# Performance work log

Hardware: AMD Instinct MI355X
Metric: run time of the kernel (lower is better)

## Reference

```python
import jax, jax.numpy as jnp
import numpy as np

ALPHA = 0.2        # LeakyReLU negative slope
NEG = -9e15        # mask value used by the torch module
N, FIN, H, D = 4096, 20, 4, 64


def gat_layer(h, adj_mask, W, a_src, a_dst, average):
    """Multi-head GAT layer. W: [H,Fin,Fout], a_src/a_dst: [H,Fout].
    e_ij = LeakyReLU(a_src . Wh_i + a_dst . Wh_j) == a^T [Wh_i || Wh_j],
    identical math to the N x N x 2F concat in the torch code, without
    materializing the pairwise concat tensor."""
    Wh = jnp.einsum('nf,hfo->hno', h, W)                 # [H,N,F]
    f_s = jnp.einsum('hno,ho->hn', Wh, a_src)            # [H,N]
    f_d = jnp.einsum('hno,ho->hn', Wh, a_dst)            # [H,N]
    e = jax.nn.leaky_relu(f_s[:, :, None] + f_d[:, None, :], ALPHA)  # [H,N,N]
    e = jnp.where(adj_mask[None], e, NEG)
    att = jax.nn.softmax(e, axis=-1)
    out = jax.nn.elu(jnp.einsum('hnm,hmo->hno', att, Wh))  # per-head ELU (concat=True inside)
    if average:
        return out.mean(axis=0)                           # [N,F]
    return jnp.transpose(out, (1, 0, 2)).reshape(h.shape[0], -1)  # [N,H*F]


def setup_inputs() -> dict:
    key = jax.random.key(0)
    ks = jax.random.split(key, 6)
    x = jax.random.normal(ks[0], (N, FIN), jnp.float32)
    adj = jax.random.randint(ks[1], (N, N), 0, 2, jnp.int32)
    # layer 0: 20 -> 64 per head, 4 heads, concat -> 256
    W0 = jax.random.normal(ks[2], (H, FIN, D), jnp.float32) * 0.3
    a0 = jax.random.normal(ks[3], (H, 2 * D), jnp.float32) * 0.1
    # layer 1: 256 -> 64 per head, heads averaged
    W1 = jax.random.normal(ks[4], (H, H * D, D), jnp.float32) * 0.06
    a1 = jax.random.normal(ks[5], (H, 2 * D), jnp.float32) * 0.1
    return {"x": x, "adj": adj, "W0": W0, "a0": a0, "W1": W1, "a1": a1}


def reference(x, adj, W0, a0, W1, a1):
    mask = adj > 0
    h = gat_layer(x, mask, W0, a0[:, :D], a0[:, D:], average=False)   # [N, 256]
    return gat_layer(h, mask, W1, a1[:, :D], a1[:, D:], average=True)  # [N, 64]
```

## Files before the change

### kernel.cpp

```cpp
#include <hip/hip_runtime.h>
#include <hip/hip_fp16.h>
#include <math.h>

#define NN 4096
#define FIN 20
#define NH 4
#define DH 64
#define ALPHA 0.2f
#define LOG2E 1.4426950408889634f

typedef _Float16 f16x8 __attribute__((ext_vector_type(8)));
typedef _Float16 f16x4 __attribute__((ext_vector_type(4)));
typedef __fp16 fp16x2 __attribute__((ext_vector_type(2)));
typedef float f32x4 __attribute__((ext_vector_type(4)));

#if defined(__has_builtin)
#if __has_builtin(__builtin_amdgcn_exp2f)
#define FEXP2(x) __builtin_amdgcn_exp2f(x)
#endif
#endif
#ifndef FEXP2
extern "C" __device__ float __ocml_native_exp2_f32(float);
#define FEXP2(x) __ocml_native_exp2_f32(x)
#endif

__device__ inline void gload_lds16(const void* gsrc, void* ldsbase) {
    __builtin_amdgcn_global_load_lds(
        (const __attribute__((address_space(1))) void*)gsrc,
        (__attribute__((address_space(3))) void*)ldsbase, 16, 0, 0);
}

__global__ __launch_bounds__(256) void k_pack(const int* __restrict__ adj,
        unsigned char* __restrict__ bits) {
    int t = blockIdx.x * 256 + threadIdx.x;
    const int4* p = (const int4*)(adj + (size_t)t * 8);
    int4 a = p[0], b = p[1];
    unsigned int byte = 0;
    byte |= (a.x > 0) << 0; byte |= (a.y > 0) << 1;
    byte |= (a.z > 0) << 2; byte |= (a.w > 0) << 3;
    byte |= (b.x > 0) << 4; byte |= (b.y > 0) << 5;
    byte |= (b.z > 0) << 6; byte |= (b.w > 0) << 7;
    bits[t] = (unsigned char)byte;
}

__global__ __launch_bounds__(256) void k_l0wh(const float* __restrict__ x,
        const float* __restrict__ W0, const float* __restrict__ a0,
        _Float16* __restrict__ whT, float* __restrict__ fs, float* __restrict__ fd) {
    __shared__ float xs[16 * FIN];
    int n0 = blockIdx.x * 16;
    int tid = threadIdx.x;
    for (int i = tid; i < 16 * FIN; i += 256) xs[i] = x[n0 * FIN + i];
    __syncthreads();
    int h = tid >> 6, d = tid & 63;
    float w0r[FIN];
#pragma unroll
    for (int f = 0; f < FIN; ++f) w0r[f] = W0[(h * FIN + f) * DH + d];
    float asrc = a0[h * 2 * DH + d];
    float adst = a0[h * 2 * DH + DH + d];
    f16x8 wv[2];
#pragma unroll
    for (int n = 0; n < 16; ++n) {
        float wh = 0.f;
#pragma unroll
        for (int f = 0; f < FIN; ++f) wh = fmaf(xs[n * FIN + f], w0r[f], wh);
        wv[n >> 3][n & 7] = (_Float16)wh;
        float sv = wh * asrc, dv = wh * adst;
#pragma unroll
        for (int off = 1; off <= 32; off <<= 1) {
            sv += __shfl_xor(sv, off);
            dv += __shfl_xor(dv, off);
        }
        if (d == 0) { fs[h * NN + n0 + n] = sv; fd[h * NN + n0 + n] = dv; }
    }
    _Float16* dst = whT + ((size_t)(h * DH + d) * NN + n0);
    *(f16x8*)(dst) = wv[0];
    *(f16x8*)(dst + 8) = wv[1];
}

__global__ __launch_bounds__(256) void k_fdmax(const float* __restrict__ fd,
        float* __restrict__ fdm) {
    int h = blockIdx.x, tid = threadIdx.x;
    float m = -3e38f;
    for (int i = tid; i < NN; i += 256) m = fmaxf(m, fd[h * NN + i]);
#pragma unroll
    for (int off = 1; off <= 32; off <<= 1) m = fmaxf(m, __shfl_xor(m, off));
    __shared__ float mx[4];
    if ((tid & 63) == 0) mx[tid >> 6] = m;
    __syncthreads();
    if (tid == 0) fdm[h] = fmaxf(fmaxf(mx[0], mx[1]), fmaxf(mx[2], mx[3]));
}

__global__ void k_w1t(const float* __restrict__ W1, _Float16* __restrict__ w1T) {
    int u = blockIdx.x * 256 + threadIdx.x;
    int h = u >> 14, f = (u >> 6) & 255, d = u & 63;
    w1T[((size_t)(h * DH + d) << 8) + f] = (_Float16)W1[u];
}

__global__ __launch_bounds__(512) void k_attn(const float* __restrict__ fs,
        const float* __restrict__ fd, const float* __restrict__ fdmax,
        const _Float16* __restrict__ whT, const unsigned char* __restrict__ bits,
        float* __restrict__ pv, float* __restrict__ pl) {
    __shared__ __align__(16) char smem[34304];
    const int ch = blockIdx.x & 1;
    const int rowblk = (blockIdx.x >> 1) & 63;
    const int h = blockIdx.x >> 7;
    const int row0 = rowblk << 6;
    const int cb0 = ch << 11;
    const int tid = threadIdx.x;
    const int l = tid & 63, w = tid >> 6;
    const int rl = l & 15, g = l >> 4;
    const int rg = w >> 2, cq = w & 3;
    const int r0 = row0 + rg * 32 + rl;
    const int r1 = r0 + 16;
    const float fsr0 = fs[h * NN + r0], fsr1 = fs[h * NN + r1];
    const float fm = fdmax[h];
    const float su0 = fsr0 + fm, su1 = fsr1 + fm;
    const float m0 = fmaxf(su0, ALPHA * su0);
    const float m1 = fmaxf(su1, ALPHA * su1);
    const float A0 = (fsr0 - m0) * LOG2E, B0 = (ALPHA * fsr0 - m0) * LOG2E;
    const float A1 = (fsr1 - m1) * LOG2E, B1 = (ALPHA * fsr1 - m1) * LOG2E;
    const float* fdp = fd + h * NN + cb0 + cq * 32 + g * 8;
    const unsigned char* bp0 = bits + (size_t)r0 * (NN / 8) + (cb0 >> 3) + cq * 4;
    const unsigned char* bp1 = bits + (size_t)r1 * (NN / 8) + (cb0 >> 3) + cq * 4;
    const _Float16* whb = whT + (size_t)h * DH * NN + cb0;

    const int d0_ = tid >> 4, c0_ = tid & 15;
    const int d1_ = 32 + (tid >> 4), c1_ = tid & 15;
    const _Float16* src0 = whb + (size_t)d0_ * NN + 8 * (c0_ ^ (d0_ & 15));
    const _Float16* src1 = whb + (size_t)d1_ * NN + 8 * (c1_ ^ (d1_ & 15));
    char* dstA0 = smem + w * 1024;
    char* dstA1 = smem + 8192 + w * 1024;
    char* dstB0 = smem + 16384 + w * 1024;
    char* dstB1 = smem + 16384 + 8192 + w * 1024;

    f32x4 acc0[4] = {{0,0,0,0},{0,0,0,0},{0,0,0,0},{0,0,0,0}};
    f32x4 acc1[4] = {{0,0,0,0},{0,0,0,0},{0,0,0,0},{0,0,0,0}};
    f32x4 al0 = {0,0,0,0}, al1 = {0,0,0,0};
    f16x8 ones;
#pragma unroll
    for (int i = 0; i < 8; ++i) ones[i] = (_Float16)1.0f;
    const int rdswz = ((((cq << 2) | g) ^ rl) << 4);

    gload_lds16(src0, dstA0);
    gload_lds16(src1, dstA1);
    float4 faA = *(const float4*)(fdp);
    float4 fbA = *(const float4*)(fdp + 4);
    unsigned int mA0 = *(const unsigned int*)(bp0);
    unsigned int mA1 = *(const unsigned int*)(bp1);
    float4 faB, fbB;
    unsigned int mB0, mB1;
    __syncthreads();

#define COMPUTE(BUF, FA, FB, M0v, M1v)                                          \
    {                                                                           \
        const float fv[8] = {FA.x, FA.y, FA.z, FA.w, FB.x, FB.y, FB.z, FB.w};   \
        f16x8 av0, av1;                                                         \
        const int sh = g << 3;                                                  \
        _Pragma("unroll")                                                       \
        for (int i = 0; i < 8; i += 2) {                                        \
            float ta = fmaxf(fmaf(fv[i], LOG2E, A0), fmaf(fv[i], ALPHA * LOG2E, B0)); \
            ta = ((M0v >> (sh + i)) & 1u) ? ta : -1e30f;                        \
            float tb = fmaxf(fmaf(fv[i+1], LOG2E, A0), fmaf(fv[i+1], ALPHA * LOG2E, B0)); \
            tb = ((M0v >> (sh + i + 1)) & 1u) ? tb : -1e30f;                    \
            fp16x2 p0 = __builtin_amdgcn_cvt_pkrtz(FEXP2(ta), FEXP2(tb));       \
            av0[i] = (_Float16)p0[0]; av0[i+1] = (_Float16)p0[1];               \
            float tc = fmaxf(fmaf(fv[i], LOG2E, A1), fmaf(fv[i], ALPHA * LOG2E, B1)); \
            tc = ((M1v >> (sh + i)) & 1u) ? tc : -1e30f;                        \
            float td = fmaxf(fmaf(fv[i+1], LOG2E, A1), fmaf(fv[i+1], ALPHA * LOG2E, B1)); \
            td = ((M1v >> (sh + i + 1)) & 1u) ? td : -1e30f;                    \
            fp16x2 p1 = __builtin_amdgcn_cvt_pkrtz(FEXP2(tc), FEXP2(td));       \
            av1[i] = (_Float16)p1[0]; av1[i+1] = (_Float16)p1[1];               \
        }                                                                       \
        al0 = __builtin_amdgcn_mfma_f32_16x16x32_f16(av0, ones, al0, 0, 0, 0);  \
        al1 = __builtin_amdgcn_mfma_f32_16x16x32_f16(av1, ones, al1, 0, 0, 0);  \
        _Pragma("unroll")                                                       \
        for (int t4 = 0; t4 < 4; ++t4) {                                        \
            f16x8 bv = *(const f16x8*)((BUF) + ((16 * t4 + rl) << 8) + rdswz);  \
            acc0[t4] = __builtin_amdgcn_mfma_f32_16x16x32_f16(av0, bv, acc0[t4], 0, 0, 0); \
            acc1[t4] = __builtin_amdgcn_mfma_f32_16x16x32_f16(av1, bv, acc1[t4], 0, 0, 0); \
        }                                                                       \
    }

#pragma unroll 1
    for (int k = 0; k < 8; ++k) {
        const int tB = 2 * k + 1;
        gload_lds16(src0 + tB * 128, dstB0);
        gload_lds16(src1 + tB * 128, dstB1);
        faB = *(const float4*)(fdp + tB * 128);
        fbB = *(const float4*)(fdp + tB * 128 + 4);
        mB0 = *(const unsigned int*)(bp0 + tB * 16);
        mB1 = *(const unsigned int*)(bp1 + tB * 16);
        COMPUTE(smem, faA, fbA, mA0, mA1);
        __syncthreads();
        if (k < 7) {
            const int tA = 2 * k + 2;
            gload_lds16(src0 + tA * 128, dstA0);
            gload_lds16(src1 + tA * 128, dstA1);
            faA = *(const float4*)(fdp + tA * 128);
            fbA = *(const float4*)(fdp + tA * 128 + 4);
            mA0 = *(const unsigned int*)(bp0 + tA * 16);
            mA1 = *(const unsigned int*)(bp1 + tA * 16);
        }
        COMPUTE((smem + 16384), faB, fbB, mB0, mB1);
        __syncthreads();
    }
#undef COMPUTE

    float* red = (float*)smem;
    float* lred = (float*)(smem + 33792);
#pragma unroll
    for (int p = 0; p < 2; ++p) {
        if (rg == p) {
#pragma unroll
            for (int t4 = 0; t4 < 4; ++t4)
#pragma unroll
                for (int i = 0; i < 4; ++i) {
                    red[(cq * 32 + 4 * g + i) * 66 + 16 * t4 + rl]      = acc0[t4][i];
                    red[(cq * 32 + 16 + 4 * g + i) * 66 + 16 * t4 + rl] = acc1[t4][i];
                }
            if (rl == 0) {
#pragma unroll
                for (int i = 0; i < 4; ++i) {
                    lred[cq * 32 + 4 * g + i]      = al0[i];
                    lred[cq * 32 + 16 + 4 * g + i] = al1[i];
                }
            }
        }
        __syncthreads();
#pragma unroll
        for (int j = 0; j < 4; ++j) {
            const int R = w * 4 + j;
            float v = 0.f, L = 0.f;
#pragma unroll
            for (int cc = 0; cc < 4; ++cc) {
                v += red[(cc * 32 + R) * 66 + l];
                L += lred[cc * 32 + R];
            }
            const int Rg = row0 + p * 32 + R;
            pv[(((size_t)(ch * NH + h) * NN) + Rg) * 64 + l] = v;
            if (l == 0) pl[(size_t)(ch * NH + h) * NN + Rg] = L;
        }
        __syncthreads();
    }
}

template<int MODE>
__global__ __launch_bounds__(256) void k_merge(const float* __restrict__ pv,
        const float* __restrict__ pl, void* __restrict__ outp) {
    int t = blockIdx.x * 256 + threadIdx.x;
    if (MODE == 0) {
        int d = t & 63, n = (t >> 6) & (NN - 1), h = t >> 18;
        float v = pv[((size_t)h * NN + n) * 64 + d] + pv[((size_t)(NH + h) * NN + n) * 64 + d];
        float L = pl[h * NN + n] + pl[NH * NN + h * NN + n];
        float o = v * __builtin_amdgcn_rcpf(L);
        o = o > 0.f ? o : __expf(o) - 1.f;
        ((_Float16*)outp)[(size_t)n * (NH * DH) + h * DH + d] = (_Float16)o;
    } else {
        int d = t & 63, n = t >> 6;
        float s = 0.f;
#pragma unroll
        for (int h = 0; h < NH; ++h) {
            float v = pv[((size_t)h * NN + n) * 64 + d] + pv[((size_t)(NH + h) * NN + n) * 64 + d];
            float L = pl[h * NN + n] + pl[NH * NN + h * NN + n];
            float o = v * __builtin_amdgcn_rcpf(L);
            s += o > 0.f ? o : __expf(o) - 1.f;
        }
        ((float*)outp)[t] = 0.25f * s;
    }
}

__global__ __launch_bounds__(256) void k_l1wh(const _Float16* __restrict__ h16,
        const _Float16* __restrict__ w1T, const float* __restrict__ a1,
        _Float16* __restrict__ whT, float* __restrict__ fs, float* __restrict__ fd) {
    __shared__ float red[4][16][64];
    __shared__ _Float16 lt[16][64];
    int h = blockIdx.x >> 8;
    int row0 = (blockIdx.x & 255) << 4;
    int tid = threadIdx.x;
    int l = tid & 63, w = tid >> 6;
    int rl = l & 15, g = l >> 4;
    f32x4 acc[4] = {{0,0,0,0},{0,0,0,0},{0,0,0,0},{0,0,0,0}};
    const _Float16* ap = h16 + (size_t)(row0 + rl) * (NH * DH) + w * 64;
    const _Float16* bp = w1T + ((size_t)h * DH << 8) + w * 64;
#pragma unroll
    for (int j = 0; j < 2; ++j) {
        int fb = j * 32 + 8 * g;
        f16x8 avv = *(const f16x8*)(ap + fb);
#pragma unroll
        for (int t4 = 0; t4 < 4; ++t4) {
            f16x8 bv = *(const f16x8*)(bp + ((size_t)(16 * t4 + rl) << 8) + fb);
            acc[t4] = __builtin_amdgcn_mfma_f32_16x16x32_f16(avv, bv, acc[t4], 0, 0, 0);
        }
    }
#pragma unroll
    for (int t4 = 0; t4 < 4; ++t4)
#pragma unroll
        for (int i = 0; i < 4; ++i) red[w][t4 * 4 + i][l] = acc[t4][i];
    __syncthreads();
#pragma unroll
    for (int i = 0; i < 4; ++i) {
        float v = red[0][w * 4 + i][l] + red[1][w * 4 + i][l]
                + red[2][w * 4 + i][l] + red[3][w * 4 + i][l];
        lt[4 * g + i][16 * w + rl] = (_Float16)v;
    }
    __syncthreads();
    int d = tid & 63, rb = tid >> 6;
    f16x4 o;
#pragma unroll
    for (int j = 0; j < 4; ++j) o[j] = lt[rb * 4 + j][d];
    *(f16x4*)(whT + (size_t)(h * DH + d) * NN + row0 + rb * 4) = o;
    float as_ = a1[h * 2 * DH + d], ad_ = a1[h * 2 * DH + DH + d];
    float svj[4], dvj[4];
#pragma unroll
    for (int j = 0; j < 4; ++j) {
        float wv = (float)lt[rb * 4 + j][d];
        svj[j] = wv * as_;
        dvj[j] = wv * ad_;
    }
#pragma unroll
    for (int off = 1; off <= 32; off <<= 1) {
#pragma unroll
        for (int j = 0; j < 4; ++j) {
            svj[j] += __shfl_xor(svj[j], off);
            dvj[j] += __shfl_xor(dvj[j], off);
        }
    }
    if (d == 0) {
#pragma unroll
        for (int j = 0; j < 4; ++j) {
            fs[h * NN + row0 + rb * 4 + j] = svj[j];
            fd[h * NN + row0 + rb * 4 + j] = dvj[j];
        }
    }
}

extern "C" void kernel_launch(void* const* d_in, const int* in_sizes, int n_in,
                              void* d_out, int out_size, void* d_ws, size_t ws_size,
                              hipStream_t stream) {
    const float* x  = (const float*)d_in[0];
    const int* adj  = (const int*)d_in[1];
    const float* W0 = (const float*)d_in[2];
    const float* a0 = (const float*)d_in[3];
    const float* W1 = (const float*)d_in[4];
    const float* a1 = (const float*)d_in[5];
    float* out = (float*)d_out;
    char* ws = (char*)d_ws;

    unsigned char* bits = (unsigned char*)(ws);
    _Float16* whT0 = (_Float16*)(ws + (2ull << 20));
    _Float16* h16  = (_Float16*)(ws + (4ull << 20));
    _Float16* w1T  = (_Float16*)(ws + (6ull << 20));
    _Float16* whT1 = (_Float16*)(ws + (6ull << 20) + (256ull << 10));
    float* fs0  = (float*)(ws + (9ull << 20));
    float* fd0  = fs0 + NH * NN;
    float* fs1  = fd0 + NH * NN;
    float* fd1  = fs1 + NH * NN;
    float* fdm0 = fd1 + NH * NN;
    float* fdm1 = fdm0 + 8;
    float* pv   = (float*)(ws + (10ull << 20));
    float* pl   = (float*)(ws + (18ull << 20));

    k_pack<<<NN * NN / 8 / 256, 256, 0, stream>>>(adj, bits);
    k_w1t<<<(NH * NH * DH * DH) / 256, 256, 0, stream>>>(W1, w1T);
    k_l0wh<<<NN / 16, 256, 0, stream>>>(x, W0, a0, whT0, fs0, fd0);
    k_fdmax<<<NH, 256, 0, stream>>>(fd0, fdm0);
    k_attn<<<2 * NH * (NN / 64), 512, 0, stream>>>(fs0, fd0, fdm0, whT0, bits, pv, pl);
    k_merge<0><<<(NH * NN * DH) / 256, 256, 0, stream>>>(pv, pl, h16);
    k_l1wh<<<NH * (NN / 16), 256, 0, stream>>>(h16, w1T, a1, whT1, fs1, fd1);
    k_fdmax<<<NH, 256, 0, stream>>>(fd1, fdm1);
    k_attn<<<2 * NH * (NN / 64), 512, 0, stream>>>(fs1, fd1, fdm1, whT1, bits, pv, pl);
    k_merge<1><<<(NN * DH) / 256, 256, 0, stream>>>(pv, pl, out);
}
```

Measured before the change: 110.8 us.

## Split attention columns four ways and fuse front-end kernels into one launch

After: 128.1 us. 1.16x slower.

```diff
diff --git a/kernel.cpp b/kernel.cpp
--- a/kernel.cpp
+++ b/kernel.cpp
@@ -30,51 +30,57 @@
         (__attribute__((address_space(3))) void*)ldsbase, 16, 0, 0);
 }
 
-__global__ __launch_bounds__(256) void k_pack(const int* __restrict__ adj,
-        unsigned char* __restrict__ bits) {
-    int t = blockIdx.x * 256 + threadIdx.x;
-    const int4* p = (const int4*)(adj + (size_t)t * 8);
-    int4 a = p[0], b = p[1];
-    unsigned int byte = 0;
-    byte |= (a.x > 0) << 0; byte |= (a.y > 0) << 1;
-    byte |= (a.z > 0) << 2; byte |= (a.w > 0) << 3;
-    byte |= (b.x > 0) << 4; byte |= (b.y > 0) << 5;
-    byte |= (b.z > 0) << 6; byte |= (b.w > 0) << 7;
-    bits[t] = (unsigned char)byte;
-}
-
-__global__ __launch_bounds__(256) void k_l0wh(const float* __restrict__ x,
+__global__ __launch_bounds__(256) void k_front(const int* __restrict__ adj,
+        unsigned char* __restrict__ bits, const float* __restrict__ x,
         const float* __restrict__ W0, const float* __restrict__ a0,
-        _Float16* __restrict__ whT, float* __restrict__ fs, float* __restrict__ fd) {
+        _Float16* __restrict__ whT, float* __restrict__ fs, float* __restrict__ fd,
+        const float* __restrict__ W1, _Float16* __restrict__ w1T) {
     __shared__ float xs[16 * FIN];
-    int n0 = blockIdx.x * 16;
-    int tid = threadIdx.x;
-    for (int i = tid; i < 16 * FIN; i += 256) xs[i] = x[n0 * FIN + i];
-    __syncthreads();
-    int h = tid >> 6, d = tid & 63;
-    float w0r[FIN];
-#pragma unroll
-    for (int f = 0; f < FIN; ++f) w0r[f] = W0[(h * FIN + f) * DH + d];
-    float asrc = a0[h * 2 * DH + d];
-    float adst = a0[h * 2 * DH + DH + d];
-    f16x8 wv[2];
-#pragma unroll
-    for (int n = 0; n < 16; ++n) {
-        float wh = 0.f;
-#pragma unroll
-        for (int f = 0; f < FIN; ++f) wh = fmaf(xs[n * FIN + f], w0r[f], wh);
-        wv[n >> 3][n & 7] = (_Float16)wh;
-        float sv = wh * asrc, dv = wh * adst;
-#pragma unroll
-        for (int off = 1; off <= 32; off <<= 1) {
-            sv += __shfl_xor(sv, off);
-            dv += __shfl_xor(dv, off);
-        }
-        if (d == 0) { fs[h * NN + n0 + n] = sv; fd[h * NN + n0 + n] = dv; }
-    }
-    _Float16* dst = whT + ((size_t)(h * DH + d) * NN + n0);
-    *(f16x8*)(dst) = wv[0];
-    *(f16x8*)(dst + 8) = wv[1];
+    const int bid = blockIdx.x;
+    const int tid = threadIdx.x;
+    if (bid < 8192) {
+        int t = bid * 256 + tid;
+        const int4* p = (const int4*)(adj + (size_t)t * 8);
+        int4 a = p[0], b = p[1];
+        unsigned int byte = 0;
+        byte |= (a.x > 0) << 0; byte |= (a.y > 0) << 1;
+        byte |= (a.z > 0) << 2; byte |= (a.w > 0) << 3;
+        byte |= (b.x > 0) << 4; byte |= (b.y > 0) << 5;
+        byte |= (b.z > 0) << 6; byte |= (b.w > 0) << 7;
+        bits[t] = (unsigned char)byte;
+    } else if (bid < 8448) {
+        int n0 = (bid - 8192) * 16;
+        for (int i = tid; i < 16 * FIN; i += 256) xs[i] = x[n0 * FIN + i];
+        __syncthreads();
+        int h = tid >> 6, d = tid & 63;
+        float w0r[FIN];
+#pragma unroll
+        for (int f = 0; f < FIN; ++f) w0r[f] = W0[(h * FIN + f) * DH + d];
+        float asrc = a0[h * 2 * DH + d];
+        float adst = a0[h * 2 * DH + DH + d];
+        f16x8 wv[2];
+#pragma unroll
+        for (int n = 0; n < 16; ++n) {
+            float wh = 0.f;
+#pragma unroll
+            for (int f = 0; f < FIN; ++f) wh = fmaf(xs[n * FIN + f], w0r[f], wh);
+            wv[n >> 3][n & 7] = (_Float16)wh;
+            float sv = wh * asrc, dv = wh * adst;
+#pragma unroll
+            for (int off = 1; off <= 32; off <<= 1) {
+                sv += __shfl_xor(sv, off);
+                dv += __shfl_xor(dv, off);
+            }
+            if (d == 0) { fs[h * NN + n0 + n] = sv; fd[h * NN + n0 + n] = dv; }
+        }
+        _Float16* dst = whT + ((size_t)(h * DH + d) * NN + n0);
+        *(f16x8*)(dst) = wv[0];
+        *(f16x8*)(dst + 8) = wv[1];
+    } else {
+        int u = (bid - 8448) * 256 + tid;
+        int h = u >> 14, f = (u >> 6) & 255, d = u & 63;
+        w1T[((size_t)(h * DH + d) << 8) + f] = (_Float16)W1[u];
+    }
 }
 
 __global__ __launch_bounds__(256) void k_fdmax(const float* __restrict__ fd,
@@ -90,22 +96,16 @@
     if (tid == 0) fdm[h] = fmaxf(fmaxf(mx[0], mx[1]), fmaxf(mx[2], mx[3]));
 }
 
-__global__ void k_w1t(const float* __restrict__ W1, _Float16* __restrict__ w1T) {
-    int u = blockIdx.x * 256 + threadIdx.x;
-    int h = u >> 14, f = (u >> 6) & 255, d = u & 63;
-    w1T[((size_t)(h * DH + d) << 8) + f] = (_Float16)W1[u];
-}
-
 __global__ __launch_bounds__(512) void k_attn(const float* __restrict__ fs,
         const float* __restrict__ fd, const float* __restrict__ fdmax,
         const _Float16* __restrict__ whT, const unsigned char* __restrict__ bits,
         float* __restrict__ pv, float* __restrict__ pl) {
     __shared__ __align__(16) char smem[34304];
-    const int ch = blockIdx.x & 1;
-    const int rowblk = (blockIdx.x >> 1) & 63;
-    const int h = blockIdx.x >> 7;
+    const int ck = blockIdx.x & 3;
+    const int rowblk = (blockIdx.x >> 2) & 63;
+    const int h = blockIdx.x >> 8;
     const int row0 = rowblk << 6;
-    const int cb0 = ch << 11;
+    const int cb0 = ck << 10;
     const int tid = threadIdx.x;
     const int l = tid & 63, w = tid >> 6;
     const int rl = l & 15, g = l >> 4;
@@ -182,7 +182,7 @@
     }
 
 #pragma unroll 1
-    for (int k = 0; k < 8; ++k) {
+    for (int k = 0; k < 4; ++k) {
         const int tB = 2 * k + 1;
         gload_lds16(src0 + tB * 128, dstB0);
         gload_lds16(src1 + tB * 128, dstB1);
@@ -192,7 +192,7 @@
         mB1 = *(const unsigned int*)(bp1 + tB * 16);
         COMPUTE(smem, faA, fbA, mA0, mA1);
         __syncthreads();
-        if (k < 7) {
+        if (k < 3) {
             const int tA = 2 * k + 2;
             gload_lds16(src0 + tA * 128, dstA0);
             gload_lds16(src1 + tA * 128, dstA1);
@@ -237,8 +237,8 @@
                 L += lred[cc * 32 + R];
             }
             const int Rg = row0 + p * 32 + R;
-            pv[(((size_t)(ch * NH + h) * NN) + Rg) * 64 + l] = v;
-            if (l == 0) pl[(size_t)(ch * NH + h) * NN + Rg] = L;
+            pv[(((size_t)(ck * NH + h) * NN) + Rg) * 64 + l] = v;
+            if (l == 0) pl[(size_t)(ck * NH + h) * NN + Rg] = L;
         }
         __syncthreads();
     }
@@ -250,8 +250,12 @@
     int t = blockIdx.x * 256 + threadIdx.x;
     if (MODE == 0) {
         int d = t & 63, n = (t >> 6) & (NN - 1), h = t >> 18;
-        float v = pv[((size_t)h * NN + n) * 64 + d] + pv[((size_t)(NH + h) * NN + n) * 64 + d];
-        float L = pl[h * NN + n] + pl[NH * NN + h * NN + n];
+        float v = 0.f, L = 0.f;
+#pragma unroll
+        for (int cc = 0; cc < 4; ++cc) {
+            v += pv[(((size_t)(cc * NH + h) * NN) + n) * 64 + d];
+            L += pl[(size_t)(cc * NH + h) * NN + n];
+        }
         float o = v * __builtin_amdgcn_rcpf(L);
         o = o > 0.f ? o : __expf(o) - 1.f;
         ((_Float16*)outp)[(size_t)n * (NH * DH) + h * DH + d] = (_Float16)o;
@@ -260,8 +264,12 @@
         float s = 0.f;
 #pragma unroll
         for (int h = 0; h < NH; ++h) {
-            float v = pv[((size_t)h * NN + n) * 64 + d] + pv[((size_t)(NH + h) * NN + n) * 64 + d];
-            float L = pl[h * NN + n] + pl[NH * NN + h * NN + n];
+            float v = 0.f, L = 0.f;
+#pragma unroll
+            for (int cc = 0; cc < 4; ++cc) {
+                v += pv[(((size_t)(cc * NH + h) * NN) + n) * 64 + d];
+                L += pl[(size_t)(cc * NH + h) * NN + n];
+            }
             float o = v * __builtin_amdgcn_rcpf(L);
             s += o > 0.f ? o : __expf(o) - 1.f;
         }
@@ -358,16 +366,14 @@
     float* fdm0 = fd1 + NH * NN;
     float* fdm1 = fdm0 + 8;
     float* pv   = (float*)(ws + (10ull << 20));
-    float* pl   = (float*)(ws + (18ull << 20));
-
-    k_pack<<<NN * NN / 8 / 256, 256, 0, stream>>>(adj, bits);
-    k_w1t<<<(NH * NH * DH * DH) / 256, 256, 0, stream>>>(W1, w1T);
-    k_l0wh<<<NN / 16, 256, 0, stream>>>(x, W0, a0, whT0, fs0, fd0);
+    float* pl   = (float*)(ws + (26ull << 20));
+
+    k_front<<<8704, 256, 0, stream>>>(adj, bits, x, W0, a0, whT0, fs0, fd0, W1, w1T);
     k_fdmax<<<NH, 256, 0, stream>>>(fd0, fdm0);
-    k_attn<<<2 * NH * (NN / 64), 512, 0, stream>>>(fs0, fd0, fdm0, whT0, bits, pv, pl);
+    k_attn<<<4 * NH * (NN / 64), 512, 0, stream>>>(fs0, fd0, fdm0, whT0, bits, pv, pl);
     k_merge<0><<<(NH * NN * DH) / 256, 256, 0, stream>>>(pv, pl, h16);
     k_l1wh<<<NH * (NN / 16), 256, 0, stream>>>(h16, w1T, a1, whT1, fs1, fd1);
     k_fdmax<<<NH, 256, 0, stream>>>(fd1, fdm1);
-    k_attn<<<2 * NH * (NN / 64), 512, 0, stream>>>(fs1, fd1, fdm1, whT1, bits, pv, pl);
+    k_attn<<<4 * NH * (NN / 64), 512, 0, stream>>>(fs1, fd1, fdm1, whT1, bits, pv, pl);
     k_merge<1><<<(NN * DH) / 256, 256, 0, stream>>>(pv, pl, out);
 }
```
